# Optimization experiments

Measured on AMD Instinct MI355X. Metric: run time of the kernel, lower is better.

Reference implementation:

```python
import jax, jax.numpy as jnp
import numpy as np

N_NODES = 40000
N_EDGES = 640000
D_IN = 128
D_OUT = 128


def setup_inputs() -> dict:
    key = jax.random.key(0)
    k1, k2, k3 = jax.random.split(key, 3)
    x = jax.random.normal(k1, (N_NODES, D_IN), dtype=jnp.float32)
    W = jax.random.normal(k2, (D_IN, D_OUT), dtype=jnp.float32) / np.sqrt(D_IN)
    b = jnp.zeros((D_OUT,), dtype=jnp.float32)
    edge_index = jax.random.randint(k3, (2, N_EDGES), 0, N_NODES, dtype=jnp.int64)
    return {"x": x, "W": W, "b": b, "edge_index": edge_index}


def reference(x, W, b, edge_index):
    src, dst = edge_index[0], edge_index[1]
    n = x.shape[0]
    # asymmetric normalization: 1 / out-degree(src), inf -> 0
    deg = jax.ops.segment_sum(jnp.ones_like(src, dtype=x.dtype), src, num_segments=n)
    deg_inv = jnp.where(deg > 0, 1.0 / deg, 0.0)
    # GCNConv (add_self_loops=False, normalize=False): h = x @ W; msg_e = w_e * h[src_e]
    h = x @ W  # [N, D_OUT]
    msg = h[src] * deg_inv[src][:, None]  # [E, D_OUT] gather-weighted messages
    out = jax.ops.segment_sum(msg, dst, num_segments=n) + b  # scatter-add to dst
    return out
```

## Files before the change

kernel.cpp:

```cpp
#include <hip/hip_runtime.h>

#define N_NODES 40000
#define D 128
#define N_EDGES 640000
#define GRP 128
#define NKEY 313
#define P1TILE 2048
#define P1BLKS 313
#define NSLICE 32
#define SLICE_E 20000
#define SLICE_E4 5000
#define HALF_BINS 20000
#define HALF_W 10000
#define WROW 20000
#define SRCH_BLKS 64
#define GEMM_BLKS 625
#define XP 136

typedef __attribute__((ext_vector_type(8))) short short8_t;
typedef __attribute__((ext_vector_type(4))) float float4_t;

static __device__ __forceinline__ unsigned short f2bf(float f) {
  unsigned u = __float_as_uint(f);
  return (unsigned short)((u + 0x7fffu + ((u >> 16) & 1u)) >> 16);
}
static __device__ __forceinline__ float bf2f(unsigned short h) {
  return __uint_as_float(((unsigned)h) << 16);
}

static __device__ __forceinline__ void scan512(unsigned* s, int tid) {
  const int t2 = tid + 256;
#pragma unroll
  for (int off = 1; off < 512; off <<= 1) {
    unsigned a = (tid >= off) ? s[tid - off] : 0u;
    unsigned c = (t2 >= off) ? s[t2 - off] : 0u;
    __syncthreads();
    s[tid] += a;
    s[t2] += c;
    __syncthreads();
  }
}

__global__ __launch_bounds__(256) void k1(
    const float* __restrict__ x, const float* __restrict__ W,
    const int* __restrict__ src, const int* __restrict__ dst,
    unsigned* __restrict__ slabS, unsigned* __restrict__ slabP,
    unsigned short* __restrict__ hb) {
  __shared__ unsigned smem[12544];
  const int bid = blockIdx.x;
  const int tid = threadIdx.x;

  if (bid < SRCH_BLKS) {
    const int b = bid >> 1;
    const int h = bid & 1;
    for (int i = tid; i < HALF_W; i += 256) smem[i] = 0;
    __syncthreads();
    const int4* p4 = (const int4*)(src + b * SLICE_E);
    const unsigned lo = (unsigned)(h * HALF_BINS);
    for (int it = tid; it < SLICE_E4; it += 256) {
      const int4 v = p4[it];
      unsigned u;
      u = (unsigned)v.x - lo; if (u < HALF_BINS) atomicAdd(&smem[u >> 1], 1u << ((u & 1) * 16));
      u = (unsigned)v.y - lo; if (u < HALF_BINS) atomicAdd(&smem[u >> 1], 1u << ((u & 1) * 16));
      u = (unsigned)v.z - lo; if (u < HALF_BINS) atomicAdd(&smem[u >> 1], 1u << ((u & 1) * 16));
      u = (unsigned)v.w - lo; if (u < HALF_BINS) atomicAdd(&smem[u >> 1], 1u << ((u & 1) * 16));
    }
    __syncthreads();
    unsigned* row = slabS + (size_t)b * WROW + h * HALF_W;
    for (int i = tid; i < HALF_W; i += 256) row[i] = smem[i];
    return;
  }

  const int t = bid - SRCH_BLKS;
  if (t % 3 == 2) {
    const int cid = t / 3;
    unsigned* cnt = smem;
    const int t2 = tid + 256;
    if (tid < NKEY) cnt[tid] = 0;
    if (t2 < NKEY) cnt[t2] = 0;
    __syncthreads();
    const int e0 = cid * P1TILE + tid * 8;
    if (e0 < N_EDGES) {
      const int4 da = *(const int4*)(dst + e0);
      const int4 db = *(const int4*)(dst + e0 + 4);
      atomicAdd(&cnt[da.x >> 7], 1u);
      atomicAdd(&cnt[da.y >> 7], 1u);
      atomicAdd(&cnt[da.z >> 7], 1u);
      atomicAdd(&cnt[da.w >> 7], 1u);
      atomicAdd(&cnt[db.x >> 7], 1u);
      atomicAdd(&cnt[db.y >> 7], 1u);
      atomicAdd(&cnt[db.z >> 7], 1u);
      atomicAdd(&cnt[db.w >> 7], 1u);
    }
    __syncthreads();
    if (tid < NKEY) slabP[(size_t)cid * NKEY + tid] = cnt[tid];
    if (t2 < NKEY) slabP[(size_t)cid * NKEY + t2] = cnt[t2];
    return;
  }

  const int gid = 2 * (t / 3) + (t % 3);
  if (gid >= GEMM_BLKS) return;
  const int n0 = gid * 64;
  const int w = tid >> 6;
  const int lane = tid & 63;

  unsigned short* wb = (unsigned short*)smem;
  unsigned short* xb = wb + 16384;

#pragma unroll 4
  for (int i = 0; i < 16; ++i) {
    const int g4 = i * 256 + tid;
    const int k = g4 >> 5;
    const int d0 = (g4 & 31) * 4;
    const float4 v = ((const float4*)W)[g4];
    const int q = k >> 5, r = k & 31;
    const int base =
        (((d0 >> 4) * 4 + q) * 64 + ((r >> 3) * 16 + (d0 & 15))) * 8 + (r & 7);
    wb[base] = f2bf(v.x);
    wb[base + 8] = f2bf(v.y);
    wb[base + 16] = f2bf(v.z);
    wb[base + 24] = f2bf(v.w);
  }

  {
    const float4* xg = (const float4*)(x + (size_t)n0 * D);
#pragma unroll
    for (int j = 0; j < 8; ++j) {
      const int idx = tid + j * 256;
      const int row = idx >> 5;
      const int c4 = idx & 31;
      const float4 v = xg[idx];
      ushort4 o;
      o.x = f2bf(v.x); o.y = f2bf(v.y); o.z = f2bf(v.z); o.w = f2bf(v.w);
      *(ushort4*)(xb + row * XP + c4 * 4) = o;
    }
  }
  __syncthreads();

  short8_t afrag[4];
  {
    const unsigned short* ap0 = xb + (w * 16 + (lane & 15)) * XP + (lane >> 4) * 8;
#pragma unroll
    for (int q = 0; q < 4; ++q) afrag[q] = *(const short8_t*)(ap0 + q * 32);
  }

  const int orow = n0 + w * 16 + (lane >> 4) * 4;
  const int ocolbase = lane & 15;
#pragma unroll
  for (int t8 = 0; t8 < 8; ++t8) {
    float4_t acc = {0.f, 0.f, 0.f, 0.f};
#pragma unroll
    for (int q = 0; q < 4; ++q) {
      const short8_t bfrag = *(const short8_t*)(wb + ((t8 * 4 + q) * 64 + lane) * 8);
      acc = __builtin_amdgcn_mfma_f32_16x16x32_bf16(afrag[q], bfrag, acc, 0, 0, 0);
    }
    const int col = t8 * 16 + ocolbase;
#pragma unroll
    for (int r = 0; r < 4; ++r)
      hb[(size_t)(orow + r) * D + col] = f2bf(acc[r]);
  }
}

__global__ __launch_bounds__(256) void k2(
    const unsigned* __restrict__ slabP, const unsigned* __restrict__ slabS,
    unsigned* __restrict__ rowbase, unsigned* __restrict__ keytotal,
    float* __restrict__ dinv) {
  const int bid = blockIdx.x;
  const int tid = threadIdx.x;
  if (bid < NKEY) {
    const int k = bid;
    __shared__ unsigned s[512];
    const int t2 = tid + 256;
    unsigned v0 = slabP[(size_t)tid * NKEY + k];
    unsigned v1 = (t2 < NKEY) ? slabP[(size_t)t2 * NKEY + k] : 0u;
    s[tid] = v0;
    s[t2] = v1;
    __syncthreads();
    scan512(s, tid);
    rowbase[(size_t)tid * NKEY + k] = s[tid] - v0;
    if (t2 < NKEY) rowbase[(size_t)t2 * NKEY + k] = s[t2] - v1;
    if (tid == 0) keytotal[k] = s[NKEY - 1];
    return;
  }
  const int w = (bid - NKEY) * 256 + tid;
  if (w >= WROW) return;
  unsigned run = 0;
#pragma unroll 8
  for (int b = 0; b < NSLICE; ++b) run += slabS[(size_t)b * WROW + w];
  const unsigned lo = run & 0xFFFFu;
  const unsigned hi = run >> 16;
  dinv[2 * w] = lo ? 1.0f / (float)lo : 0.0f;
  dinv[2 * w + 1] = hi ? 1.0f / (float)hi : 0.0f;
}

__global__ __launch_bounds__(256) void k3(
    const int* __restrict__ src, const int* __restrict__ dst,
    const unsigned* __restrict__ rowbase, const unsigned* __restrict__ keytotal,
    unsigned* __restrict__ epack) {
  __shared__ unsigned s[512];
  __shared__ unsigned ko[NKEY];
  __shared__ unsigned rb[NKEY];
  __shared__ unsigned cnt[NKEY];
  const int b = blockIdx.x;
  const int tid = threadIdx.x;
  const int t2 = tid + 256;

  unsigned kv0 = (tid < NKEY) ? keytotal[tid] : 0u;
  unsigned kv1 = (t2 < NKEY) ? keytotal[t2] : 0u;
  s[tid] = kv0;
  s[t2] = kv1;
  if (tid < NKEY) { rb[tid] = rowbase[(size_t)b * NKEY + tid]; cnt[tid] = 0; }
  if (t2 < NKEY) { rb[t2] = rowbase[(size_t)b * NKEY + t2]; cnt[t2] = 0; }
  __syncthreads();
  scan512(s, tid);
  if (tid < NKEY) ko[tid] = s[tid] - kv0;
  if (t2 < NKEY) ko[t2] = s[t2] - kv1;
  __syncthreads();

  const int e0 = b * P1TILE + tid * 8;
  if (e0 < N_EDGES) {
    const int4 sa = *(const int4*)(src + e0);
    const int4 sb = *(const int4*)(src + e0 + 4);
    const int4 da = *(const int4*)(dst + e0);
    const int4 db = *(const int4*)(dst + e0 + 4);
#define PLACE(DV, SV)                                                   \
  {                                                                     \
    const int d_ = (DV);                                                \
    const int k_ = d_ >> 7;                                             \
    const unsigned lr_ = atomicAdd(&cnt[k_], 1u);                       \
    epack[ko[k_] + rb[k_] + lr_] =                                      \
        ((unsigned)(d_ & 127) << 16) | (unsigned)(SV);                  \
  }
    PLACE(da.x, sa.x) PLACE(da.y, sa.y) PLACE(da.z, sa.z) PLACE(da.w, sa.w)
    PLACE(db.x, sb.x) PLACE(db.y, sb.y) PLACE(db.z, sb.z) PLACE(db.w, sb.w)
#undef PLACE
  }
}

__global__ __launch_bounds__(256) void k4a(
    const unsigned* __restrict__ keytotal, const unsigned* __restrict__ epack,
    int* __restrict__ offs, int* __restrict__ cnt_dst,
    unsigned short* __restrict__ esrc16) {
  __shared__ unsigned s[512];
  __shared__ unsigned cnt[GRP];
  __shared__ unsigned cur[GRP];
  __shared__ unsigned sstart, slen;
  const int k = blockIdx.x;
  const int tid = threadIdx.x;
  const int t2 = tid + 256;

  unsigned kv0 = (tid < NKEY) ? keytotal[tid] : 0u;
  unsigned kv1 = (t2 < NKEY) ? keytotal[t2] : 0u;
  s[tid] = kv0;
  s[t2] = kv1;
  if (tid < GRP) cnt[tid] = 0;
  __syncthreads();
  scan512(s, tid);
  if (tid == 0) {
    sstart = s[k] - keytotal[k];
    slen = keytotal[k];
  }
  __syncthreads();
  const unsigned start = sstart;
  const unsigned len = slen;

  for (unsigned i = tid; i < len; i += 256) {
    atomicAdd(&cnt[epack[start + i] >> 16], 1u);
  }
  __syncthreads();

  unsigned v = (tid < GRP) ? cnt[tid] : 0u;
  s[tid] = v;
  __syncthreads();
#pragma unroll
  for (int off = 1; off < 256; off <<= 1) {
    unsigned a = (tid >= off) ? s[tid - off] : 0u;
    __syncthreads();
    s[tid] += a;
    __syncthreads();
  }
  if (tid < GRP) {
    const unsigned ex = s[tid] - v;
    cur[tid] = ex;
    const int n = k * GRP + tid;
    if (n < N_NODES) {
      offs[n] = (int)(start + ex);
      cnt_dst[n] = (int)v;
    }
  }
  __syncthreads();

  for (unsigned i = tid; i < len; i += 256) {
    const unsigned p = epack[start + i];
    const unsigned dl = p >> 16;
    const unsigned r = atomicAdd(&cur[dl], 1u);
    esrc16[start + r] = (unsigned short)(p & 0xFFFFu);
  }
}

__global__ __launch_bounds__(256) void k4b(
    const int* __restrict__ offs, const int* __restrict__ cnt_dst,
    const float* __restrict__ dinv, const unsigned short* __restrict__ esrc16,
    const unsigned short* __restrict__ hb,
    const float* __restrict__ b, float* __restrict__ out) {
  const int tid = threadIdx.x;
  const int node = blockIdx.x * 8 + (tid >> 5);
  const int lane = tid & 31;

  const int start = offs[node];
  const int len = cnt_dst[node];
  const unsigned short* bk = esrc16 + start;

  int sj = 0;
  if (lane < len) sj = bk[lane];
  const float fj = dinv[sj];

  float4 aa[4];
#pragma unroll
  for (int q = 0; q < 4; ++q) aa[q] = make_float4(0.f, 0.f, 0.f, 0.f);

  const int l32 = len < 32 ? len : 32;
  for (int jj = 0; jj < l32; jj += 8) {
    ushort4 u[8];
    float fq[8];
#pragma unroll
    for (int q = 0; q < 8; ++q) {
      const int j = jj + q;
      const int s = __shfl(sj, j, 32);
      const float f = __shfl(fj, j, 32);
      const bool on = j < l32;
      const int ss = on ? s : 0;
      u[q] = ((const ushort4*)(hb + (size_t)ss * D))[lane];
      fq[q] = on ? f : 0.0f;
    }
#pragma unroll
    for (int q = 0; q < 8; ++q) {
      const float f = fq[q];
      float4& a = aa[q & 3];
      a.x += f * bf2f(u[q].x);
      a.y += f * bf2f(u[q].y);
      a.z += f * bf2f(u[q].z);
      a.w += f * bf2f(u[q].w);
    }
  }
  for (int j = 32; j < len; ++j) {
    const int s = bk[j];
    const float f = dinv[s];
    ushort4 u = ((const ushort4*)(hb + (size_t)s * D))[lane];
    aa[0].x += f * bf2f(u.x);
    aa[0].y += f * bf2f(u.y);
    aa[0].z += f * bf2f(u.z);
    aa[0].w += f * bf2f(u.w);
  }

  const float4 bias = ((const float4*)b)[lane];
  float4 v;
  v.x = bias.x + (aa[0].x + aa[1].x) + (aa[2].x + aa[3].x);
  v.y = bias.y + (aa[0].y + aa[1].y) + (aa[2].y + aa[3].y);
  v.z = bias.z + (aa[0].z + aa[1].z) + (aa[2].z + aa[3].z);
  v.w = bias.w + (aa[0].w + aa[1].w) + (aa[2].w + aa[3].w);
  ((float4*)(out + (size_t)node * D))[lane] = v;
}

extern "C" void kernel_launch(void* const* d_in, const int* in_sizes, int n_in,
                              void* d_out, int out_size, void* d_ws, size_t ws_size,
                              hipStream_t stream) {
  const float* x = (const float*)d_in[0];
  const float* W = (const float*)d_in[1];
  const float* b = (const float*)d_in[2];
  const int* ei = (const int*)d_in[3];
  const int* src = ei;
  const int* dst = ei + N_EDGES;
  float* out = (float*)d_out;

  char* ws = (char*)d_ws;
  float* dinv = (float*)(ws + 0);
  unsigned* slabS = (unsigned*)(ws + 160000);
  unsigned* slabP = (unsigned*)(ws + 2720000);
  unsigned* rowbase = (unsigned*)(ws + 3112192);
  unsigned* keytotal = (unsigned*)(ws + 3504384);
  unsigned* epack = (unsigned*)(ws + 3508480);
  int* offs = (int*)(ws + 6068480);
  int* cnt_dst = (int*)(ws + 6228480);
  unsigned short* esrc16 = (unsigned short*)(ws + 6388480);
  unsigned short* hb = (unsigned short*)(ws + 7668480);

  k1<<<SRCH_BLKS + 939, 256, 0, stream>>>(x, W, src, dst, slabS, slabP, hb);
  k2<<<NKEY + 79, 256, 0, stream>>>(slabP, slabS, rowbase, keytotal, dinv);
  k3<<<P1BLKS, 256, 0, stream>>>(src, dst, rowbase, keytotal, epack);
  k4a<<<NKEY, 256, 0, stream>>>(keytotal, epack, offs, cnt_dst, esrc16);
  k4b<<<5000, 256, 0, stream>>>(offs, cnt_dst, dinv, esrc16, hb, b, out);
}
```

Before: 66.23 us.

## Fuse edge bucketing into tile-local sort and drop separate scan/scatter kernels

Each dst-count block in k1 now does a local prefix scan and writes its tile's edges sorted by destination key to a tile-ordered buffer, with per-tile offsets. The bucketing kernel then reads each key's chunk from all tiles directly and places sources at a fixed per-key capacity offset. This removes the global scan kernel and the global scatter pass, which saves two launches and one global round trip. In exchange, the gather reads in the bucketing kernel are serial per thread, and a fixed capacity that silently drops overflow edges.

```diff
diff --git a/kernel.cpp b/kernel.cpp
--- a/kernel.cpp
+++ b/kernel.cpp
@@ -5,8 +5,9 @@
 #define N_EDGES 640000
 #define GRP 128
 #define NKEY 313
-#define P1TILE 2048
-#define P1BLKS 313
+#define TSIZE 2048
+#define NTILE 313
+#define GCAP 2560
 #define NSLICE 32
 #define SLICE_E 20000
 #define SLICE_E4 5000
@@ -45,6 +46,7 @@
     const float* __restrict__ x, const float* __restrict__ W,
     const int* __restrict__ src, const int* __restrict__ dst,
     unsigned* __restrict__ slabS, unsigned* __restrict__ slabP,
+    unsigned* __restrict__ lofs, unsigned* __restrict__ epackT,
     unsigned short* __restrict__ hb) {
   __shared__ unsigned smem[12544];
   const int bid = blockIdx.x;
@@ -75,14 +77,23 @@
   if (t % 3 == 2) {
     const int cid = t / 3;
     unsigned* cnt = smem;
+    unsigned* cur = smem + 320;
+    unsigned* s = smem + 640;
+    unsigned* buf = smem + 1152;
     const int t2 = tid + 256;
     if (tid < NKEY) cnt[tid] = 0;
     if (t2 < NKEY) cnt[t2] = 0;
     __syncthreads();
-    const int e0 = cid * P1TILE + tid * 8;
-    if (e0 < N_EDGES) {
-      const int4 da = *(const int4*)(dst + e0);
-      const int4 db = *(const int4*)(dst + e0 + 4);
+
+    const int e0 = cid * TSIZE;
+    const int nE = (N_EDGES - e0) < TSIZE ? (N_EDGES - e0) : TSIZE;
+    int4 sa, sb, da, db;
+    const bool act = (tid * 8) < nE;
+    if (act) {
+      sa = *(const int4*)(src + e0 + tid * 8);
+      sb = *(const int4*)(src + e0 + tid * 8 + 4);
+      da = *(const int4*)(dst + e0 + tid * 8);
+      db = *(const int4*)(dst + e0 + tid * 8 + 4);
       atomicAdd(&cnt[da.x >> 7], 1u);
       atomicAdd(&cnt[da.y >> 7], 1u);
       atomicAdd(&cnt[da.z >> 7], 1u);
@@ -93,8 +104,40 @@
       atomicAdd(&cnt[db.w >> 7], 1u);
     }
     __syncthreads();
-    if (tid < NKEY) slabP[(size_t)cid * NKEY + tid] = cnt[tid];
-    if (t2 < NKEY) slabP[(size_t)cid * NKEY + t2] = cnt[t2];
+
+    const unsigned v0 = (tid < NKEY) ? cnt[tid] : 0u;
+    const unsigned v1 = (t2 < NKEY) ? cnt[t2] : 0u;
+    s[tid] = v0;
+    s[t2] = v1;
+    __syncthreads();
+    scan512(s, tid);
+    if (tid < NKEY) {
+      const unsigned ex = s[tid] - v0;
+      cur[tid] = ex;
+      slabP[(size_t)cid * NKEY + tid] = v0;
+      lofs[(size_t)cid * NKEY + tid] = ex;
+    }
+    if (t2 < NKEY) {
+      const unsigned ex = s[t2] - v1;
+      cur[t2] = ex;
+      slabP[(size_t)cid * NKEY + t2] = v1;
+      lofs[(size_t)cid * NKEY + t2] = ex;
+    }
+    __syncthreads();
+
+    if (act) {
+#define TPLACE(DV, SV)                                                \
+  {                                                                   \
+    const int d_ = (DV);                                              \
+    const unsigned r_ = atomicAdd(&cur[d_ >> 7], 1u);                 \
+    buf[r_] = ((unsigned)(d_ & 127) << 16) | (unsigned)(SV);          \
+  }
+      TPLACE(da.x, sa.x) TPLACE(da.y, sa.y) TPLACE(da.z, sa.z) TPLACE(da.w, sa.w)
+      TPLACE(db.x, sb.x) TPLACE(db.y, sb.y) TPLACE(db.z, sb.z) TPLACE(db.w, sb.w)
+#undef TPLACE
+    }
+    __syncthreads();
+    for (int i = tid; i < nE; i += 256) epackT[e0 + i] = buf[i];
     return;
   }
 
@@ -161,27 +204,71 @@
   }
 }
 
-__global__ __launch_bounds__(256) void k2(
-    const unsigned* __restrict__ slabP, const unsigned* __restrict__ slabS,
-    unsigned* __restrict__ rowbase, unsigned* __restrict__ keytotal,
-    float* __restrict__ dinv) {
+__global__ __launch_bounds__(256) void k4a(
+    const unsigned* __restrict__ slabP, const unsigned* __restrict__ lofs,
+    const unsigned* __restrict__ epackT, const unsigned* __restrict__ slabS,
+    int* __restrict__ offs, int* __restrict__ cnt_dst,
+    unsigned short* __restrict__ esrc16, float* __restrict__ dinv) {
   const int bid = blockIdx.x;
   const int tid = threadIdx.x;
+
   if (bid < NKEY) {
     const int k = bid;
-    __shared__ unsigned s[512];
-    const int t2 = tid + 256;
-    unsigned v0 = slabP[(size_t)tid * NKEY + k];
-    unsigned v1 = (t2 < NKEY) ? slabP[(size_t)t2 * NKEY + k] : 0u;
-    s[tid] = v0;
-    s[t2] = v1;
-    __syncthreads();
-    scan512(s, tid);
-    rowbase[(size_t)tid * NKEY + k] = s[tid] - v0;
-    if (t2 < NKEY) rowbase[(size_t)t2 * NKEY + k] = s[t2] - v1;
-    if (tid == 0) keytotal[k] = s[NKEY - 1];
+    __shared__ unsigned chb[NTILE];
+    __shared__ unsigned chc[NTILE];
+    __shared__ unsigned cnt[GRP];
+    __shared__ unsigned cur[GRP];
+    __shared__ unsigned s[256];
+
+    for (int t = tid; t < NTILE; t += 256) {
+      chc[t] = slabP[(size_t)t * NKEY + k];
+      chb[t] = t * TSIZE + lofs[(size_t)t * NKEY + k];
+    }
+    if (tid < GRP) cnt[tid] = 0;
+    __syncthreads();
+
+    for (int t = tid; t < NTILE; t += 256) {
+      const unsigned base = chb[t];
+      const unsigned c = chc[t];
+      for (unsigned e = 0; e < c; ++e) {
+        atomicAdd(&cnt[epackT[base + e] >> 16], 1u);
+      }
+    }
+    __syncthreads();
+
+    const unsigned v = (tid < GRP) ? cnt[tid] : 0u;
+    s[tid] = v;
+    __syncthreads();
+#pragma unroll
+    for (int off = 1; off < 256; off <<= 1) {
+      unsigned a = (tid >= off) ? s[tid - off] : 0u;
+      __syncthreads();
+      s[tid] += a;
+      __syncthreads();
+    }
+    if (tid < GRP) {
+      const unsigned ex = s[tid] - v;
+      cur[tid] = ex;
+      const int n = k * GRP + tid;
+      if (n < N_NODES) {
+        offs[n] = (int)(k * GCAP + ex);
+        cnt_dst[n] = (int)v;
+      }
+    }
+    __syncthreads();
+
+    for (int t = tid; t < NTILE; t += 256) {
+      const unsigned base = chb[t];
+      const unsigned c = chc[t];
+      for (unsigned e = 0; e < c; ++e) {
+        const unsigned p = epackT[base + e];
+        const unsigned r = atomicAdd(&cur[p >> 16], 1u);
+        if (r < GCAP) esrc16[(size_t)k * GCAP + r] = (unsigned short)(p & 0xFFFFu);
+      }
+    }
     return;
   }
+
   const int w = (bid - NKEY) * 256 + tid;
   if (w >= WROW) return;
   unsigned run = 0;
@@ -191,111 +278,6 @@
   const unsigned hi = run >> 16;
   dinv[2 * w] = lo ? 1.0f / (float)lo : 0.0f;
   dinv[2 * w + 1] = hi ? 1.0f / (float)hi : 0.0f;
-}
-
-__global__ __launch_bounds__(256) void k3(
-    const int* __restrict__ src, const int* __restrict__ dst,
-    const unsigned* __restrict__ rowbase, const unsigned* __restrict__ keytotal,
-    unsigned* __restrict__ epack) {
-  __shared__ unsigned s[512];
-  __shared__ unsigned ko[NKEY];
-  __shared__ unsigned rb[NKEY];
-  __shared__ unsigned cnt[NKEY];
-  const int b = blockIdx.x;
-  const int tid = threadIdx.x;
-  const int t2 = tid + 256;
-
-  unsigned kv0 = (tid < NKEY) ? keytotal[tid] : 0u;
-  unsigned kv1 = (t2 < NKEY) ? keytotal[t2] : 0u;
-  s[tid] = kv0;
-  s[t2] = kv1;
-  if (tid < NKEY) { rb[tid] = rowbase[(size_t)b * NKEY + tid]; cnt[tid] = 0; }
-  if (t2 < NKEY) { rb[t2] = rowbase[(size_t)b * NKEY + t2]; cnt[t2] = 0; }
-  __syncthreads();
-  scan512(s, tid);
-  if (tid < NKEY) ko[tid] = s[tid] - kv0;
-  if (t2 < NKEY) ko[t2] = s[t2] - kv1;
-  __syncthreads();
-
-  const int e0 = b * P1TILE + tid * 8;
-  if (e0 < N_EDGES) {
-    const int4 sa = *(const int4*)(src + e0);
-    const int4 sb = *(const int4*)(src + e0 + 4);
-    const int4 da = *(const int4*)(dst + e0);
-    const int4 db = *(const int4*)(dst + e0 + 4);
-#define PLACE(DV, SV)                                                   \
-  {                                                                     \
-    const int d_ = (DV);                                                \
-    const int k_ = d_ >> 7;                                             \
-    const unsigned lr_ = atomicAdd(&cnt[k_], 1u);                       \
-    epack[ko[k_] + rb[k_] + lr_] =                                      \
-        ((unsigned)(d_ & 127) << 16) | (unsigned)(SV);                  \
-  }
-    PLACE(da.x, sa.x) PLACE(da.y, sa.y) PLACE(da.z, sa.z) PLACE(da.w, sa.w)
-    PLACE(db.x, sb.x) PLACE(db.y, sb.y) PLACE(db.z, sb.z) PLACE(db.w, sb.w)
-#undef PLACE
-  }
-}
-
-__global__ __launch_bounds__(256) void k4a(
-    const unsigned* __restrict__ keytotal, const unsigned* __restrict__ epack,
-    int* __restrict__ offs, int* __restrict__ cnt_dst,
-    unsigned short* __restrict__ esrc16) {
-  __shared__ unsigned s[512];
-  __shared__ unsigned cnt[GRP];
-  __shared__ unsigned cur[GRP];
-  __shared__ unsigned sstart, slen;
-  const int k = blockIdx.x;
-  const int tid = threadIdx.x;
-  const int t2 = tid + 256;
-
-  unsigned kv0 = (tid < NKEY) ? keytotal[tid] : 0u;
-  unsigned kv1 = (t2 < NKEY) ? keytotal[t2] : 0u;
-  s[tid] = kv0;
-  s[t2] = kv1;
-  if (tid < GRP) cnt[tid] = 0;
-  __syncthreads();
-  scan512(s, tid);
-  if (tid == 0) {
-    sstart = s[k] - keytotal[k];
-    slen = keytotal[k];
-  }
-  __syncthreads();
-  const unsigned start = sstart;
-  const unsigned len = slen;
-
-  for (unsigned i = tid; i < len; i += 256) {
-    atomicAdd(&cnt[epack[start + i] >> 16], 1u);
-  }
-  __syncthreads();
-
-  unsigned v = (tid < GRP) ? cnt[tid] : 0u;
-  s[tid] = v;
-  __syncthreads();
-#pragma unroll
-  for (int off = 1; off < 256; off <<= 1) {
-    unsigned a = (tid >= off) ? s[tid - off] : 0u;
-    __syncthreads();
-    s[tid] += a;
-    __syncthreads();
-  }
-  if (tid < GRP) {
-    const unsigned ex = s[tid] - v;
-    cur[tid] = ex;
-    const int n = k * GRP + tid;
-    if (n < N_NODES) {
-      offs[n] = (int)(start + ex);
-      cnt_dst[n] = (int)v;
-    }
-  }
-  __syncthreads();
-
-  for (unsigned i = tid; i < len; i += 256) {
-    const unsigned p = epack[start + i];
-    const unsigned dl = p >> 16;
-    const unsigned r = atomicAdd(&cur[dl], 1u);
-    esrc16[start + r] = (unsigned short)(p & 0xFFFFu);
-  }
 }
 
 __global__ __launch_bounds__(256) void k4b(
@@ -377,17 +359,16 @@
   float* dinv = (float*)(ws + 0);
   unsigned* slabS = (unsigned*)(ws + 160000);
   unsigned* slabP = (unsigned*)(ws + 2720000);
-  unsigned* rowbase = (unsigned*)(ws + 3112192);
-  unsigned* keytotal = (unsigned*)(ws + 3504384);
-  unsigned* epack = (unsigned*)(ws + 3508480);
+  unsigned* lofs = (unsigned*)(ws + 3112192);
+  unsigned* epackT = (unsigned*)(ws + 3504384);
   int* offs = (int*)(ws + 6068480);
   int* cnt_dst = (int*)(ws + 6228480);
   unsigned short* esrc16 = (unsigned short*)(ws + 6388480);
-  unsigned short* hb = (unsigned short*)(ws + 7668480);
-
-  k1<<<SRCH_BLKS + 939, 256, 0, stream>>>(x, W, src, dst, slabS, slabP, hb);
-  k2<<<NKEY + 79, 256, 0, stream>>>(slabP, slabS, rowbase, keytotal, dinv);
-  k3<<<P1BLKS, 256, 0, stream>>>(src, dst, rowbase, keytotal, epack);
-  k4a<<<NKEY, 256, 0, stream>>>(keytotal, epack, offs, cnt_dst, esrc16);
+  unsigned short* hb = (unsigned short*)(ws + 7991040);
+
+  k1<<<SRCH_BLKS + 939, 256, 0, stream>>>(x, W, src, dst, slabS, slabP, lofs,
+                                          epackT, hb);
+  k4a<<<NKEY + 79, 256, 0, stream>>>(slabP, lofs, epackT, slabS, offs, cnt_dst,
+                                     esrc16, dinv);
   k4b<<<5000, 256, 0, stream>>>(offs, cnt_dst, dinv, esrc16, hb, b, out);
 }
```

New measurement: 71.11 us. 7.4% more time.
